# Performance work log

Hardware: AMD Instinct MI355X
Metric: run time of the kernel (lower is better)

The kernel has to match this reference:

```python
import jax, jax.numpy as jnp
import numpy as np

WS = 8          # window_size
NH = 8          # num_heads


def rel_pos_index(ws):
    coords = jnp.stack(jnp.meshgrid(jnp.arange(ws), jnp.arange(ws), indexing='ij'))  # [2,ws,ws]
    cf = coords.reshape(2, -1)                      # [2, N]
    rc = (cf[:, :, None] - cf[:, None, :]).transpose(1, 2, 0)  # [N,N,2]
    rc = rc + (ws - 1)
    return rc[..., 0] * (2 * ws - 1) + rc[..., 1]   # [N,N] int


def setup_inputs() -> dict:
    key = jax.random.key(0)
    ks = jax.random.split(key, 10)
    dim = 256
    B_, N = 4096, WS * WS
    nW = 1024
    return {
        'ref': jax.random.normal(ks[0], (B_, N, dim), jnp.float32),
        'adj': jax.random.normal(ks[1], (B_, N, dim), jnp.float32),
        'mask': jax.random.normal(ks[2], (nW, N, N), jnp.float32),
        'q_w': jax.random.normal(ks[3], (dim, dim), jnp.float32) * 0.02,
        'q_b': jax.random.normal(ks[4], (dim,), jnp.float32) * 0.02,
        'kv_w': jax.random.normal(ks[5], (2 * dim, dim), jnp.float32) * 0.02,
        'kv_b': jax.random.normal(ks[6], (2 * dim,), jnp.float32) * 0.02,
        'proj_w': jax.random.normal(ks[7], (dim, dim), jnp.float32) * 0.02,
        'proj_b': jax.random.normal(ks[8], (dim,), jnp.float32) * 0.02,
        'rpb_table': jax.random.normal(ks[9], ((2 * WS - 1) ** 2, NH), jnp.float32) * 0.02,
        'H': 256,
        'W': 256,
    }


def reference(ref, adj, mask, q_w, q_b, kv_w, kv_b, proj_w, proj_b, rpb_table, H, W):
    B_, N, C = ref.shape
    hd = C // NH
    scale = hd ** -0.5
    # projections (torch Linear: x @ W.T + b)
    q = (ref @ q_w.T + q_b).reshape(B_, N, NH, hd).transpose(0, 2, 1, 3)    # [B_,h,N,d]
    kv = (adj @ kv_w.T + kv_b).reshape(B_, N, 2, NH, hd)
    k = kv[:, :, 0].transpose(0, 2, 1, 3)                                   # [B_,h,N,d]
    v = kv[:, :, 1].transpose(0, 2, 1, 3)
    attn = jnp.einsum('bhnd,bhmd->bhnm', q * scale, k)                      # [B_,h,N,N]
    # relative position bias gather
    rpi = rel_pos_index(WS)                                                 # [N,N]
    bias = rpb_table[rpi.reshape(-1)].reshape(N, N, NH).transpose(2, 0, 1)  # [h,N,N]
    attn = attn + bias[None]
    # shifted-window mask
    nW = (H // WS) * (W // WS)
    attn = attn.reshape(B_ // nW, nW, NH, N, N) + mask[None, :, None]
    attn = attn.reshape(B_, NH, N, N)
    attn = jax.nn.softmax(attn, axis=-1)
    out = jnp.einsum('bhnm,bhmd->bhnd', attn, v).transpose(0, 2, 1, 3).reshape(B_, N, C)
    return out @ proj_w.T + proj_b
```

## Files before the change

### kernel.cpp

```cpp
#include <hip/hip_runtime.h>

typedef unsigned short u16;
typedef unsigned int u32;
typedef float f32x4 __attribute__((ext_vector_type(4)));
typedef __bf16 bf16x8 __attribute__((ext_vector_type(8)));

__device__ __forceinline__ u32 pack2(float a, float b) {
  u32 r;
  asm("v_cvt_pk_bf16_f32 %0, %1, %2" : "=v"(r) : "v"(a), "v"(b));
  return r;
}

__device__ __forceinline__ bf16x8 xpose_tile(const f32x4 t0, const f32x4 t1,
                                             int srcA, int srcB, bool hi) {
  u32 s0 = pack2(t0[0], t0[1]);
  u32 s1 = pack2(t0[2], t0[3]);
  u32 s2 = pack2(t1[0], t1[1]);
  u32 s3 = pack2(t1[2], t1[3]);
  u32 a00 = (u32)__shfl((int)s0, srcA), a20 = (u32)__shfl((int)s2, srcA);
  u32 a01 = (u32)__shfl((int)s1, srcA), a21 = (u32)__shfl((int)s3, srcA);
  u32 b00 = (u32)__shfl((int)s0, srcB), b20 = (u32)__shfl((int)s2, srcB);
  u32 b01 = (u32)__shfl((int)s1, srcB), b21 = (u32)__shfl((int)s3, srcB);
  uint4 u;
  u.x = hi ? a20 : a00;
  u.y = hi ? a21 : a01;
  u.z = hi ? b20 : b00;
  u.w = hi ? b21 : b01;
  return __builtin_bit_cast(bf16x8, u);
}

__global__ void prep_kern(const float* __restrict__ qw_f, const float* __restrict__ kvw_f,
                          const float* __restrict__ pjw_f, const float* __restrict__ rpb,
                          const float* __restrict__ mask_g,
                          uint4* __restrict__ qwt, uint4* __restrict__ kwt,
                          uint4* __restrict__ vwt, uint4* __restrict__ pjwt,
                          float4* __restrict__ biasT, float4* __restrict__ maskT, int nW) {
  int i = blockIdx.x * 256 + threadIdx.x;
  auto wxf = [&](const float* W, int ro, int idx, uint4* dst) {
    int l = idx & 63, kk = (idx >> 6) & 7, R = idx >> 9;
    const float* s = W + (ro + R * 16 + (l & 15)) * 256 + kk * 32 + 8 * (l >> 4);
    uint4 o;
    o.x = pack2(s[0], s[1]);
    o.y = pack2(s[2], s[3]);
    o.z = pack2(s[4], s[5]);
    o.w = pack2(s[6], s[7]);
    dst[idx] = o;
  };
  if (i < 32768) {
    wxf(qw_f, 0, i, qwt);
  } else if (i < 65536) {
    wxf(kvw_f, 0, i - 32768, kwt);
  } else if (i < 98304) {
    wxf(kvw_f, 256, i - 65536, vwt);
  } else if (i < 131072) {
    wxf(pjw_f, 0, i - 98304, pjwt);
  } else if (i < 139264) {
    int j = i - 131072;
    int l = j & 63, mt = (j >> 6) & 3, nt = (j >> 8) & 3, h = j >> 10;
    int n = nt * 16 + (l & 15), m0 = mt * 16 + 4 * (l >> 4);
    float4 o;
    float* po = (float*)&o;
#pragma unroll
    for (int e = 0; e < 4; ++e) {
      int m = m0 + e;
      int rp = ((n >> 3) - (m >> 3) + 7) * 15 + ((n & 7) - (m & 7) + 7);
      po[e] = rpb[rp * 8 + h];
    }
    biasT[j] = o;
  } else {
    int k = i - 139264;
    if (k < nW * 1024) {
      int l = k & 63, mt = (k >> 6) & 3, nt = (k >> 8) & 3, wd = k >> 10;
      int n = nt * 16 + (l & 15), m0 = mt * 16 + 4 * (l >> 4);
      maskT[k] = *(const float4*)(mask_g + (size_t)wd * 4096 + n * 64 + m0);
    }
  }
}

#define XROW 528

#define K1_LDS 33792

__global__ __launch_bounds__(256, 2) void winattn_kern(
    const float* __restrict__ xr_g, const float* __restrict__ xa_g,
    const float* __restrict__ qb_g, const float* __restrict__ kvb_g,
    const float* __restrict__ pb_g,
    const uint4* __restrict__ qwt, const uint4* __restrict__ kwt,
    const uint4* __restrict__ vwt, const uint4* __restrict__ pjwt,
    const float4* __restrict__ biasT, const float4* __restrict__ maskT,
    float* __restrict__ out_g, int nW) {
  extern __shared__ char smem[];
  const int tid = threadIdx.x;
  const int l = tid & 63, wv = tid >> 6;
  const int lr = l & 15, lq = l >> 4;
  const int b = blockIdx.x;
  const int wd = b % nW;
  const float scale = 0.17677669529663687f;
  const int srcA = lr + 32 * (lq & 1);
  const int srcB = srcA + 16;
  const bool hi = (lq >> 1) != 0;

  auto stage = [&](const float* src) {
#pragma unroll 4
    for (int it = 0; it < 16; ++it) {
      int flat = it * 256 + tid;
      int t = flat >> 6, c4 = (flat & 63) << 2;
      float4 v = *(const float4*)(src + t * 256 + c4);
      uint2 w;
      w.x = pack2(v.x, v.y);
      w.y = pack2(v.z, v.w);
      *(uint2*)(smem + t * XROW + c4 * 2) = w;
    }
  };

  stage(xr_g + (size_t)b * 16384);
  __syncthreads();

  bf16x8 bfr[2][4];

  {
    f32x4 qacc[4][4];
#pragma unroll
    for (int i = 0; i < 4; ++i)
#pragma unroll
      for (int j = 0; j < 4; ++j) qacc[i][j] = {0.f, 0.f, 0.f, 0.f};
#pragma unroll 2
    for (int kk = 0; kk < 8; ++kk) {
      bf16x8 a0 = *(const bf16x8*)&qwt[((wv * 4 + 0) * 8 + kk) * 64 + l];
      bf16x8 a1 = *(const bf16x8*)&qwt[((wv * 4 + 1) * 8 + kk) * 64 + l];
      bf16x8 a2 = *(const bf16x8*)&qwt[((wv * 4 + 2) * 8 + kk) * 64 + l];
      bf16x8 a3 = *(const bf16x8*)&qwt[((wv * 4 + 3) * 8 + kk) * 64 + l];
      int c = kk * 32 + 8 * lq;
#pragma unroll
      for (int nt = 0; nt < 4; ++nt) {
        bf16x8 bt = *(const bf16x8*)(smem + (nt * 16 + lr) * XROW + c * 2);
        qacc[0][nt] = __builtin_amdgcn_mfma_f32_16x16x32_bf16(a0, bt, qacc[0][nt], 0, 0, 0);
        qacc[1][nt] = __builtin_amdgcn_mfma_f32_16x16x32_bf16(a1, bt, qacc[1][nt], 0, 0, 0);
        qacc[2][nt] = __builtin_amdgcn_mfma_f32_16x16x32_bf16(a2, bt, qacc[2][nt], 0, 0, 0);
        qacc[3][nt] = __builtin_amdgcn_mfma_f32_16x16x32_bf16(a3, bt, qacc[3][nt], 0, 0, 0);
      }
    }
#pragma unroll
    for (int rt = 0; rt < 4; ++rt) {
      float4 b4 = *(const float4*)(qb_g + wv * 64 + rt * 16 + 4 * lq);
#pragma unroll
      for (int nt = 0; nt < 4; ++nt) {
        qacc[rt][nt][0] = (qacc[rt][nt][0] + b4.x) * scale;
        qacc[rt][nt][1] = (qacc[rt][nt][1] + b4.y) * scale;
        qacc[rt][nt][2] = (qacc[rt][nt][2] + b4.z) * scale;
        qacc[rt][nt][3] = (qacc[rt][nt][3] + b4.w) * scale;
      }
    }
#pragma unroll
    for (int h2 = 0; h2 < 2; ++h2)
#pragma unroll
      for (int nt = 0; nt < 4; ++nt)
        bfr[h2][nt] = xpose_tile(qacc[2 * h2][nt], qacc[2 * h2 + 1][nt], srcA, srcB, hi);
  }
  __syncthreads();

  stage(xa_g + (size_t)b * 16384);
  __syncthreads();

  bf16x8 afr[2][4];
  {
    f32x4 kacc[4][4];
#pragma unroll
    for (int i = 0; i < 4; ++i)
#pragma unroll
      for (int j = 0; j < 4; ++j) kacc[i][j] = {0.f, 0.f, 0.f, 0.f};
#pragma unroll 2
    for (int kk = 0; kk < 8; ++kk) {
      bf16x8 a0 = *(const bf16x8*)&kwt[((wv * 4 + 0) * 8 + kk) * 64 + l];
      bf16x8 a1 = *(const bf16x8*)&kwt[((wv * 4 + 1) * 8 + kk) * 64 + l];
      bf16x8 a2 = *(const bf16x8*)&kwt[((wv * 4 + 2) * 8 + kk) * 64 + l];
      bf16x8 a3 = *(const bf16x8*)&kwt[((wv * 4 + 3) * 8 + kk) * 64 + l];
      int c = kk * 32 + 8 * lq;
#pragma unroll
      for (int nt = 0; nt < 4; ++nt) {
        bf16x8 bt = *(const bf16x8*)(smem + (nt * 16 + lr) * XROW + c * 2);
        kacc[0][nt] = __builtin_amdgcn_mfma_f32_16x16x32_bf16(a0, bt, kacc[0][nt], 0, 0, 0);
        kacc[1][nt] = __builtin_amdgcn_mfma_f32_16x16x32_bf16(a1, bt, kacc[1][nt], 0, 0, 0);
        kacc[2][nt] = __builtin_amdgcn_mfma_f32_16x16x32_bf16(a2, bt, kacc[2][nt], 0, 0, 0);
        kacc[3][nt] = __builtin_amdgcn_mfma_f32_16x16x32_bf16(a3, bt, kacc[3][nt], 0, 0, 0);
      }
    }
#pragma unroll
    for (int rt = 0; rt < 4; ++rt) {
      float4 b4 = *(const float4*)(kvb_g + wv * 64 + rt * 16 + 4 * lq);
#pragma unroll
      for (int nt = 0; nt < 4; ++nt) {
        kacc[rt][nt][0] += b4.x;
        kacc[rt][nt][1] += b4.y;
        kacc[rt][nt][2] += b4.z;
        kacc[rt][nt][3] += b4.w;
      }
    }
#pragma unroll
    for (int h2 = 0; h2 < 2; ++h2)
#pragma unroll
      for (int nt = 0; nt < 4; ++nt)
        afr[h2][nt] = xpose_tile(kacc[2 * h2][nt], kacc[2 * h2 + 1][nt], srcA, srcB, hi);
  }

  bf16x8 vfr[2][2][2];
  {
    f32x4 vacc[4][4];
#pragma unroll
    for (int i = 0; i < 4; ++i)
#pragma unroll
      for (int j = 0; j < 4; ++j) vacc[i][j] = {0.f, 0.f, 0.f, 0.f};
#pragma unroll 2
    for (int kk = 0; kk < 8; ++kk) {
      bf16x8 b0 = *(const bf16x8*)&vwt[((wv * 4 + 0) * 8 + kk) * 64 + l];
      bf16x8 b1 = *(const bf16x8*)&vwt[((wv * 4 + 1) * 8 + kk) * 64 + l];
      bf16x8 b2 = *(const bf16x8*)&vwt[((wv * 4 + 2) * 8 + kk) * 64 + l];
      bf16x8 b3 = *(const bf16x8*)&vwt[((wv * 4 + 3) * 8 + kk) * 64 + l];
      int c = kk * 32 + 8 * lq;
#pragma unroll
      for (int mt = 0; mt < 4; ++mt) {
        bf16x8 at = *(const bf16x8*)(smem + (mt * 16 + lr) * XROW + c * 2);
        vacc[mt][0] = __builtin_amdgcn_mfma_f32_16x16x32_bf16(at, b0, vacc[mt][0], 0, 0, 0);
        vacc[mt][1] = __builtin_amdgcn_mfma_f32_16x16x32_bf16(at, b1, vacc[mt][1], 0, 0, 0);
        vacc[mt][2] = __builtin_amdgcn_mfma_f32_16x16x32_bf16(at, b2, vacc[mt][2], 0, 0, 0);
        vacc[mt][3] = __builtin_amdgcn_mfma_f32_16x16x32_bf16(at, b3, vacc[mt][3], 0, 0, 0);
      }
    }
#pragma unroll
    for (int ct = 0; ct < 4; ++ct) {
      float bv = kvb_g[256 + wv * 64 + ct * 16 + lr];
#pragma unroll
      for (int mt = 0; mt < 4; ++mt)
#pragma unroll
        for (int j = 0; j < 4; ++j) vacc[mt][ct][j] += bv;
    }
#pragma unroll
    for (int h2 = 0; h2 < 2; ++h2)
#pragma unroll
      for (int kk = 0; kk < 2; ++kk)
#pragma unroll
        for (int cg = 0; cg < 2; ++cg)
          vfr[h2][kk][cg] =
              xpose_tile(vacc[2 * kk][2 * h2 + cg], vacc[2 * kk + 1][2 * h2 + cg], srcA, srcB, hi);
  }
  __syncthreads();

#pragma unroll
  for (int h2 = 0; h2 < 2; ++h2) {
    const int h = wv * 2 + h2;

    f32x4 sacc[4][4];
    {
      const float4* bT = biasT + (size_t)h * 1024;
      const float4* mT = maskT + (size_t)wd * 1024;
#pragma unroll
      for (int nt = 0; nt < 4; ++nt) {
#pragma unroll
        for (int mt = 0; mt < 4; ++mt) {
          float4 bi = bT[(nt * 4 + mt) * 64 + l];
          float4 m4 = mT[(nt * 4 + mt) * 64 + l];
          sacc[mt][nt][0] = bi.x + m4.x;
          sacc[mt][nt][1] = bi.y + m4.y;
          sacc[mt][nt][2] = bi.z + m4.z;
          sacc[mt][nt][3] = bi.w + m4.w;
        }
      }
    }
#pragma unroll
    for (int mt = 0; mt < 4; ++mt)
#pragma unroll
      for (int nt = 0; nt < 4; ++nt)
        sacc[mt][nt] = __builtin_amdgcn_mfma_f32_16x16x32_bf16(afr[h2][mt], bfr[h2][nt],
                                                               sacc[mt][nt], 0, 0, 0);

    float rden[4];
#pragma unroll
    for (int nt = 0; nt < 4; ++nt) {
      float lmx = -1e30f;
#pragma unroll
      for (int mt = 0; mt < 4; ++mt)
        lmx = fmaxf(lmx, fmaxf(fmaxf(sacc[mt][nt][0], sacc[mt][nt][1]),
                               fmaxf(sacc[mt][nt][2], sacc[mt][nt][3])));
      lmx = fmaxf(lmx, __shfl_xor(lmx, 16));
      lmx = fmaxf(lmx, __shfl_xor(lmx, 32));
      float ls = 0.f;
#pragma unroll
      for (int mt = 0; mt < 4; ++mt) {
#pragma unroll
        for (int j = 0; j < 4; ++j) {
          float e = __expf(sacc[mt][nt][j] - lmx);
          sacc[mt][nt][j] = e;
          ls += e;
        }
      }
      ls += __shfl_xor(ls, 16);
      ls += __shfl_xor(ls, 32);
      rden[nt] = 1.0f / ls;
    }

    bf16x8 pfr[2][4];
#pragma unroll
    for (int kk = 0; kk < 2; ++kk)
#pragma unroll
      for (int nt = 0; nt < 4; ++nt)
        pfr[kk][nt] = xpose_tile(sacc[2 * kk][nt], sacc[2 * kk + 1][nt], srcA, srcB, hi);

    f32x4 oacc[2][4];
#pragma unroll
    for (int i = 0; i < 2; ++i)
#pragma unroll
      for (int j = 0; j < 4; ++j) oacc[i][j] = {0.f, 0.f, 0.f, 0.f};
#pragma unroll
    for (int kk = 0; kk < 2; ++kk)
#pragma unroll
      for (int nt = 0; nt < 4; ++nt) {
        oacc[0][nt] = __builtin_amdgcn_mfma_f32_16x16x32_bf16(vfr[h2][kk][0], pfr[kk][nt],
                                                              oacc[0][nt], 0, 0, 0);
        oacc[1][nt] = __builtin_amdgcn_mfma_f32_16x16x32_bf16(vfr[h2][kk][1], pfr[kk][nt],
                                                              oacc[1][nt], 0, 0, 0);
      }

#pragma unroll
    for (int cg = 0; cg < 2; ++cg) {
      int cb = h * 32 + cg * 16 + 4 * lq;
#pragma unroll
      for (int nt = 0; nt < 4; ++nt) {
        int n = nt * 16 + lr;
        float r = rden[nt];
        uint2 w;
        w.x = pack2(oacc[cg][nt][0] * r, oacc[cg][nt][1] * r);
        w.y = pack2(oacc[cg][nt][2] * r, oacc[cg][nt][3] * r);
        *(uint2*)(smem + n * XROW + cb * 2) = w;
      }
    }
  }
  __syncthreads();

  {
    f32x4 acc[4][4];
#pragma unroll
    for (int i = 0; i < 4; ++i)
#pragma unroll
      for (int j = 0; j < 4; ++j) acc[i][j] = {0.f, 0.f, 0.f, 0.f};
#pragma unroll 2
    for (int kk = 0; kk < 8; ++kk) {
      bf16x8 w0 = *(const bf16x8*)&pjwt[((wv * 4 + 0) * 8 + kk) * 64 + l];
      bf16x8 w1 = *(const bf16x8*)&pjwt[((wv * 4 + 1) * 8 + kk) * 64 + l];
      bf16x8 w2 = *(const bf16x8*)&pjwt[((wv * 4 + 2) * 8 + kk) * 64 + l];
      bf16x8 w3 = *(const bf16x8*)&pjwt[((wv * 4 + 3) * 8 + kk) * 64 + l];
      int c = kk * 32 + 8 * lq;
#pragma unroll
      for (int mt = 0; mt < 4; ++mt) {
        bf16x8 at = *(const bf16x8*)(smem + (mt * 16 + lr) * XROW + c * 2);
        acc[mt][0] = __builtin_amdgcn_mfma_f32_16x16x32_bf16(at, w0, acc[mt][0], 0, 0, 0);
        acc[mt][1] = __builtin_amdgcn_mfma_f32_16x16x32_bf16(at, w1, acc[mt][1], 0, 0, 0);
        acc[mt][2] = __builtin_amdgcn_mfma_f32_16x16x32_bf16(at, w2, acc[mt][2], 0, 0, 0);
        acc[mt][3] = __builtin_amdgcn_mfma_f32_16x16x32_bf16(at, w3, acc[mt][3], 0, 0, 0);
      }
    }
    float* outb = out_g + (size_t)b * 16384;
#pragma unroll
    for (int rt = 0; rt < 4; ++rt) {
      int c = wv * 64 + rt * 16 + lr;
      float pbv = pb_g[c];
#pragma unroll
      for (int mt = 0; mt < 4; ++mt) {
        int t = mt * 16 + 4 * lq;
        outb[(t + 0) * 256 + c] = acc[mt][rt][0] + pbv;
        outb[(t + 1) * 256 + c] = acc[mt][rt][1] + pbv;
        outb[(t + 2) * 256 + c] = acc[mt][rt][2] + pbv;
        outb[(t + 3) * 256 + c] = acc[mt][rt][3] + pbv;
      }
    }
  }
}

extern "C" void kernel_launch(void* const* d_in, const int* in_sizes, int n_in,
                              void* d_out, int out_size, void* d_ws, size_t ws_size,
                              hipStream_t stream) {
  const float* ref = (const float*)d_in[0];
  const float* adj = (const float*)d_in[1];
  const float* mask = (const float*)d_in[2];
  const float* q_w = (const float*)d_in[3];
  const float* q_b = (const float*)d_in[4];
  const float* kv_w = (const float*)d_in[5];
  const float* kv_b = (const float*)d_in[6];
  const float* proj_w = (const float*)d_in[7];
  const float* proj_b = (const float*)d_in[8];
  const float* rpb = (const float*)d_in[9];

  int B = in_sizes[0] / 16384;
  int nW = in_sizes[2] / 4096;

  uint4* qwt = (uint4*)d_ws;
  uint4* kwt = qwt + 32768;
  uint4* vwt = kwt + 32768;
  uint4* pjwt = vwt + 32768;
  float4* biasT = (float4*)(pjwt + 32768);
  float4* maskT = biasT + 8192;

  int prep_total = 139264 + nW * 1024;
  prep_kern<<<(prep_total + 255) / 256, 256, 0, stream>>>(q_w, kv_w, proj_w, rpb, mask, qwt,
                                                          kwt, vwt, pjwt, biasT, maskT, nW);

  hipFuncSetAttribute((const void*)winattn_kern, hipFuncAttributeMaxDynamicSharedMemorySize,
                      K1_LDS);
  winattn_kern<<<B, 256, K1_LDS, stream>>>(ref, adj, q_b, kv_b, proj_b, qwt, kwt, vwt, pjwt,
                                           biasT, maskT, (float*)d_out, nW);
}
```

Baseline: 317.5 us.

## Prefetch adj tile into registers during Q projection to overlap global loads

Staging now loads each 64x256 fp32 tile into a 16-entry float4 register buffer before packing it to bf16 in shared memory. The adj tile's global loads are issued right after the ref tile is staged, so their latency overlaps the Q projection MFMA work instead of sitting behind it. The cost is 64 extra live VGPRs across the Q GEMM, which may lower occupancy or cause spills.

Measured after the change: 319.3 us. About the same (+0.5%).

```diff
diff --git a/kernel.cpp b/kernel.cpp
--- a/kernel.cpp
+++ b/kernel.cpp
@@ -100,21 +100,35 @@
   const int srcB = srcA + 16;
   const bool hi = (lq >> 1) != 0;
 
-  auto stage = [&](const float* src) {
-#pragma unroll 4
+  float4 buf[16];
+
+  {
+    const float* refb = xr_g + (size_t)b * 16384;
+#pragma unroll
+    for (int it = 0; it < 16; ++it) {
+      int flat = it * 256 + tid;
+      buf[it] = *(const float4*)(refb + (flat >> 6) * 256 + ((flat & 63) << 2));
+    }
+#pragma unroll
     for (int it = 0; it < 16; ++it) {
       int flat = it * 256 + tid;
       int t = flat >> 6, c4 = (flat & 63) << 2;
-      float4 v = *(const float4*)(src + t * 256 + c4);
       uint2 w;
-      w.x = pack2(v.x, v.y);
-      w.y = pack2(v.z, v.w);
+      w.x = pack2(buf[it].x, buf[it].y);
+      w.y = pack2(buf[it].z, buf[it].w);
       *(uint2*)(smem + t * XROW + c4 * 2) = w;
     }
-  };
-
-  stage(xr_g + (size_t)b * 16384);
+  }
   __syncthreads();
+
+  {
+    const float* adjb = xa_g + (size_t)b * 16384;
+#pragma unroll
+    for (int it = 0; it < 16; ++it) {
+      int flat = it * 256 + tid;
+      buf[it] = *(const float4*)(adjb + (flat >> 6) * 256 + ((flat & 63) << 2));
+    }
+  }
 
   bf16x8 bfr[2][4];
 
@@ -159,7 +173,17 @@
   }
   __syncthreads();
 
-  stage(xa_g + (size_t)b * 16384);
+  {
+#pragma unroll
+    for (int it = 0; it < 16; ++it) {
+      int flat = it * 256 + tid;
+      int t = flat >> 6, c4 = (flat & 63) << 2;
+      uint2 w;
+      w.x = pack2(buf[it].x, buf[it].y);
+      w.y = pack2(buf[it].z, buf[it].w);
+      *(uint2*)(smem + t * XROW + c4 * 2) = w;
+    }
+  }
   __syncthreads();
 
   bf16x8 afr[2][4];
```
